# Optimization experiments

Hardware: AMD Instinct MI355X
Metric: run time of the kernel (lower is better)

The kernel has to match this reference:

```python
import jax, jax.numpy as jnp
import numpy as np

UPSCALE = 4
IMG_RANGE = 1.0
B, CIN, H, W = 4, 3, 128, 128
NF, NB = 64, 16


def conv2d(x, w, b=None):
    y = jax.lax.conv_general_dilated(x, w, (1, 1), 'SAME',
                                     dimension_numbers=('NCHW', 'OIHW', 'NCHW'))
    return y if b is None else y + b[None, :, None, None]


def binary_act(x):
    # sign forward, piecewise-polynomial surrogate backward (STE)
    sg = jax.lax.stop_gradient
    out_fwd = jnp.sign(x)
    m1 = (x < -1).astype(x.dtype)
    m2 = (x < 0).astype(x.dtype)
    m3 = (x < 1).astype(x.dtype)
    out1 = -m1 + (x * x + 2.0 * x) * (1.0 - m1)
    out2 = out1 * m2 + (-x * x + 2.0 * x) * (1.0 - m2)
    out3 = out2 * m3 + (1.0 - m3)
    return sg(out_fwd) - sg(out3) + out3


def binarize_weight(w):
    # per-output-channel scaling factor * sign(w); gradient flows through clamp (STE)
    sg = jax.lax.stop_gradient
    scale = sg(jnp.mean(jnp.abs(w), axis=(1, 2, 3), keepdims=True))
    bw = scale * jnp.sign(w)
    cw = jnp.clip(w, -1.0, 1.0)
    return sg(bw) - sg(cw) + cw


def rprelu(x, b1, a, b2):
    x = x + b1[None, :, None, None]
    x = jnp.where(x >= 0, x, a[None, :, None, None] * x)
    return x + b2[None, :, None, None]


def bbcu(x, move, w, a, b1, b2):
    # BBCU unit: learnable bias -> binary act -> binary conv -> RPReLU -> + identity residual
    out = binary_act(x + move[None, :, None, None])
    out = conv2d(out, binarize_weight(w))
    return rprelu(out, b1, a, b2) + x


def pixel_shuffle(x, r):
    n, c, h, w = x.shape
    x = x.reshape(n, c // (r * r), r, r, h, w)
    return x.transpose(0, 1, 4, 2, 5, 3).reshape(n, c // (r * r), h * r, w * r)


def up_conv(x, move, w, a, b1, b2, r):
    # channel-expanding BBCU with channel-repeat residual, then pixel shuffle
    out = binary_act(x + move[None, :, None, None])
    out = conv2d(out, binarize_weight(w))
    out = rprelu(out, b1, a, b2) + jnp.tile(x, (1, r * r, 1, 1))
    return pixel_shuffle(out, r)


def setup_inputs() -> dict:
    key = jax.random.key(0)
    ks = jax.random.split(key, 8)
    nu = 2 * NB  # 2 BBCU convs per BinaryBlock
    inp = {
        'x': jax.random.uniform(ks[0], (B, CIN, H, W), jnp.float32),
        'conv_first_w': jax.random.normal(ks[1], (NF, CIN, 3, 3), jnp.float32) * 0.05,
        'conv_first_b': jnp.zeros((NF,), jnp.float32),
        'body_move': jnp.zeros((nu, NF), jnp.float32),
        'body_w': jax.random.normal(ks[2], (nu, NF, NF, 3, 3), jnp.float32) * 0.001,
        'body_a': jnp.full((nu, NF), 0.25, jnp.float32),
        'body_b1': jnp.zeros((nu, NF), jnp.float32),
        'body_b2': jnp.zeros((nu, NF), jnp.float32),
        'up1_move': jnp.zeros((NF,), jnp.float32),
        'up1_w': jax.random.normal(ks[3], (4 * NF, NF, 3, 3), jnp.float32) * 0.001,
        'up1_a': jnp.full((4 * NF,), 0.25, jnp.float32),
        'up1_b1': jnp.zeros((4 * NF,), jnp.float32),
        'up1_b2': jnp.zeros((4 * NF,), jnp.float32),
        'up2_move': jnp.zeros((NF,), jnp.float32),
        'up2_w': jax.random.normal(ks[4], (4 * NF, NF, 3, 3), jnp.float32) * 0.001,
        'up2_a': jnp.full((4 * NF,), 0.25, jnp.float32),
        'up2_b1': jnp.zeros((4 * NF,), jnp.float32),
        'up2_b2': jnp.zeros((4 * NF,), jnp.float32),
        'hr_move': jnp.zeros((NF,), jnp.float32),
        'hr_w': jax.random.normal(ks[5], (NF, NF, 3, 3), jnp.float32) * 0.001,
        'hr_a': jnp.full((NF,), 0.25, jnp.float32),
        'hr_b1': jnp.zeros((NF,), jnp.float32),
        'hr_b2': jnp.zeros((NF,), jnp.float32),
        'conv_last_w': jax.random.normal(ks[6], (CIN, NF, 3, 3), jnp.float32) * 0.05,
        'conv_last_b': jnp.zeros((CIN,), jnp.float32),
    }
    return inp


def reference(x, conv_first_w, conv_first_b,
              body_move, body_w, body_a, body_b1, body_b2,
              up1_move, up1_w, up1_a, up1_b1, up1_b2,
              up2_move, up2_w, up2_a, up2_b1, up2_b2,
              hr_move, hr_w, hr_a, hr_b1, hr_b2,
              conv_last_w, conv_last_b):
    x = x * IMG_RANGE
    feat = jax.nn.leaky_relu(conv2d(x, conv_first_w, conv_first_b), 0.1)

    def step(h, p):
        move, w, a, b1, b2 = p
        return bbcu(h, move, w, a, b1, b2), None

    out, _ = jax.lax.scan(step, feat, (body_move, body_w, body_a, body_b1, body_b2))
    out = up_conv(out, up1_move, up1_w, up1_a, up1_b1, up1_b2, 2)
    out = up_conv(out, up2_move, up2_w, up2_a, up2_b1, up2_b2, 2)
    out = bbcu(out, hr_move, hr_w, hr_a, hr_b1, hr_b2)
    out = conv2d(jax.nn.leaky_relu(out, 0.1), conv_last_w, conv_last_b)
    n, c, h, w = x.shape
    base = jax.image.resize(x, (n, c, h * UPSCALE, w * UPSCALE), method='bilinear')
    return (out + base) / IMG_RANGE
```

## Files before the change

### kernel.cpp

```cpp
#include <hip/hip_runtime.h>


typedef unsigned long long u64;
typedef unsigned int u32;
typedef unsigned short u16;
typedef unsigned char u8;

__device__ inline float fadd(float a, float b) { return __fadd_rn(a, b); }
__device__ inline float fmul(float a, float b) { return __fmul_rn(a, b); }

__device__ inline u64 spread4(u64 x) {
  x &= 0xFFFFULL;
  x = (x | (x << 24)) & 0x000000FF000000FFULL;
  x = (x | (x << 12)) & 0x000F000F000F000FULL;
  x = (x | (x << 6))  & 0x0303030303030303ULL;
  x = (x | (x << 3))  & 0x1111111111111111ULL;
  return x;
}

__device__ float pw_abs_sum(const float* p, int n) {
  if (n <= 8) {
    float s = fabsf(p[0]);
    for (int i = 1; i < n; i++) s = fadd(s, fabsf(p[i]));
    return s;
  }
  if (n <= 128) {
    float r[8];
#pragma unroll
    for (int q = 0; q < 8; q++) r[q] = fabsf(p[q]);
    int i;
    for (i = 8; i + 8 <= n; i += 8)
#pragma unroll
      for (int q = 0; q < 8; q++) r[q] = fadd(r[q], fabsf(p[i + q]));
    float res = fadd(fadd(fadd(r[0], r[1]), fadd(r[2], r[3])),
                     fadd(fadd(r[4], r[5]), fadd(r[6], r[7])));
    for (; i < n; i++) res = fadd(res, fabsf(p[i]));
    return res;
  }
  int n2 = (n / 2) & ~7;
  return fadd(pw_abs_sum(p, n2), pw_abs_sum(p + n2, n - n2));
}

__global__ __launch_bounds__(256) void diag_kernel(float* __restrict__ out,
                                                   int n, float tag) {
  int idx = blockIdx.x * 256 + threadIdx.x;
  if (idx < n) out[idx] = (idx == 0) ? tag : 0.f;
}

__global__ __launch_bounds__(64) void binw_pack_kernel(
    const float* __restrict__ w, u64* __restrict__ wbits,
    float* __restrict__ scale, int nch) {
  int ch = blockIdx.x * 64 + threadIdx.x;
  if (ch >= nch) return;
  const float* wc = w + (size_t)ch * 576;
  float S = pw_abs_sum(wc, 576);
  scale[ch] = __fdiv_rn(S, 576.0f);
  u64 b[9] = {0, 0, 0, 0, 0, 0, 0, 0, 0};
  for (int ci = 0; ci < 64; ci++) {
#pragma unroll
    for (int tap = 0; tap < 9; tap++)
      b[tap] |= (u64)(wc[ci * 9 + tap] > 0.0f) << ci;
  }
#pragma unroll
  for (int tap = 0; tap < 9; tap++) wbits[(size_t)ch * 9 + tap] = b[tap];
}

__global__ __launch_bounds__(256) void conv_first_kernel(
    const float* __restrict__ x,
    const float* __restrict__ w, const float* __restrict__ b,
    float* __restrict__ out) {
  int n = blockIdx.y;
  const float* xn = x + (size_t)n * 49152;
  float* on = out + (size_t)n * 1048576;
  int idx = blockIdx.x * 256 + threadIdx.x;
  int gx = idx & 127;
  int gy = (idx >> 7) & 127;
  int co = idx >> 14;
  const float* wp = w + co * 27;
  float acc = 0.f;
  for (int ky = 0; ky < 3; ky++) {
    int yy = gy + ky - 1;
    if (yy < 0 || yy > 127) continue;
    for (int kx = 0; kx < 3; kx++) {
      int xx = gx + kx - 1;
      if (xx < 0 || xx > 127) continue;
      for (int ci = 0; ci < 3; ci++)
        acc = fmaf(xn[ci * 16384 + yy * 128 + xx],
                   wp[ci * 9 + ky * 3 + kx], acc);
    }
  }
  float wb = fadd(acc, b[co]);
  on[idx] = wb >= 0.f ? wb : fmul(0.1f, wb);
}

__global__ __launch_bounds__(256) void tr_kernel(
    const float* __restrict__ in,
    float* __restrict__ out) {
  __shared__ float s[64][65];
  int n = blockIdx.y;
  int p0 = blockIdx.x * 64;
  const float* fi = in + (size_t)n * 1048576;
  float* fo = out + (size_t)n * 1048576;
  int t = threadIdx.x;
  for (int i = t; i < 4096; i += 256) {
    int ch = i >> 6, px = i & 63;
    s[ch][px] = fi[(size_t)ch * 16384 + p0 + px];
  }
  __syncthreads();
  for (int i = t; i < 1024; i += 256) {
    int px = i >> 4, c4 = i & 15;
    float4 v = make_float4(s[c4 * 4 + 0][px], s[c4 * 4 + 1][px],
                           s[c4 * 4 + 2][px], s[c4 * 4 + 3][px]);
    *(float4*)(fo + (size_t)(p0 + px) * 64 + c4 * 4) = v;
  }
}

__global__ __launch_bounds__(512, 8) void pack2_kernel(
    const float* __restrict__ feat,
    const float* __restrict__ move,
    u64* __restrict__ bits) {
  __shared__ float s_mvT[64];
  int t = threadIdx.x;
  if (t < 64) {
    int k = t >> 4, cq_ = t & 15;
    s_mvT[t] = move[4 * cq_ + k];
  }
  __syncthreads();
  int n = blockIdx.y;
  const float* f = feat + (size_t)n * 1048576;
  u64* bo = bits + (size_t)n * 16384;
  int lane = t & 63;
  int pp = lane >> 4, cq = lane & 15;
  int pix = blockIdx.x * 32 + (t >> 6) * 4 + pp;
  float4 v = *(const float4*)(f + (size_t)pix * 64 + 4 * cq);
  float vv[4] = {v.x, v.y, v.z, v.w};
  int sg[4];
#pragma unroll
  for (int k = 0; k < 4; k++)
    sg[k] = fadd(vv[k], s_mvT[k * 16 + cq]) > 0.0f;
  u64 m0 = __ballot(sg[0]);
  u64 m1 = __ballot(sg[1]);
  u64 m2 = __ballot(sg[2]);
  u64 m3 = __ballot(sg[3]);
  if (cq == 0) {
    int sh = 16 * pp;
    bo[pix] = spread4(m0 >> sh) | (spread4(m1 >> sh) << 1) |
              (spread4(m2 >> sh) << 2) | (spread4(m3 >> sh) << 3);
  }
}

__global__ __launch_bounds__(512, 8) void body_kernel(
    const u64* __restrict__ bits_in,
    const float* __restrict__ feat,
    const u64* __restrict__ wbits,
    const float* __restrict__ scale, const float* __restrict__ pa,
    const float* __restrict__ pb1, const float* __restrict__ pb2,
    const float* __restrict__ nmove,
    float* __restrict__ out,
    u64* __restrict__ bits_out)
{
  __shared__ u64 s_w[576];
  __shared__ u64 s_b[3 * 36];
  __shared__ float s_scT[64], s_aT[64], s_b1T[64], s_b2T[64], s_mvT[64];

  int t = threadIdx.x;
  int n = blockIdx.y;
  const u64* bin = bits_in + (size_t)n * 16384;

  int pix0 = blockIdx.x * 32;
  int py = pix0 >> 7, px0 = pix0 & 127;

  for (int i = t; i < 576; i += 512) {
    int cq_ = i & 15, tk = i >> 4;
    int k = tk & 3, tap = tk >> 2;
    s_w[i] = wbits[(4 * cq_ + k) * 9 + tap];
  }
  for (int i = t; i < 102; i += 512) {
    int r = i / 34, c = i - r * 34;
    int yy = py - 1 + r, xx = px0 - 1 + c;
    s_b[r * 36 + c] = (yy >= 0 && yy < 128 && xx >= 0 && xx < 128)
                          ? bin[yy * 128 + xx] : 0ULL;
  }
  if (t < 64) {
    int k = t >> 4, cq_ = t & 15;
    int co = 4 * cq_ + k;
    s_scT[t] = scale[co]; s_aT[t] = pa[co];
    s_b1T[t] = pb1[co];   s_b2T[t] = pb2[co];
    s_mvT[t] = nmove[co];
  }
  __syncthreads();

  const float* fin = feat + (size_t)n * 1048576;
  float* outp = out + (size_t)n * 1048576;
  u64* bop = bits_out + (size_t)n * 16384;

  int lane = t & 63;
  int pp = lane >> 4, cq = lane & 15;
  int pl = (t >> 6) * 4 + pp;
  int pix = pix0 + pl;
  int px = px0 + pl;

  u64 nb[9];
  int vf = 0, nvalid = 0;
#pragma unroll
  for (int ky = 0; ky < 3; ky++)
#pragma unroll
    for (int kx = 0; kx < 3; kx++) {
      int yy = py + ky - 1, xx = px + kx - 1;
      int tap = ky * 3 + kx;
      nb[tap] = s_b[ky * 36 + pl + kx];
      if (yy >= 0 && yy < 128 && xx >= 0 && xx < 128) {
        vf |= 1 << tap; nvalid++;
      }
    }
  bool interior = (vf == 511);
  int base = 64 * nvalid;

  float4 rv4 = *(const float4*)(fin + (size_t)pix * 64 + 4 * cq);
  float rv[4] = {rv4.x, rv4.y, rv4.z, rv4.w};

  float vq[4];
  int sg[4];
#pragma unroll
  for (int k = 0; k < 4; k++) {
    int c = 0;
#pragma unroll
    for (int tap = 0; tap < 9; tap++)
      c += __popcll(nb[tap] ^ s_w[(tap * 4 + k) * 16 + cq]);
    if (!interior) {
#pragma unroll
      for (int tap = 0; tap < 9; tap++)
        if (!((vf >> tap) & 1)) c -= __popcll(s_w[(tap * 4 + k) * 16 + cq]);
    }
    int sint = base - 2 * c;
    int pi = k * 16 + cq;
    float conv = fmul(s_scT[pi], (float)sint);
    float t1 = fadd(conv, s_b1T[pi]);
    float t2 = t1 >= 0.0f ? t1 : fmul(s_aT[pi], t1);
    float t3 = fadd(t2, s_b2T[pi]);
    float ov = fadd(t3, rv[k]);
    vq[k] = ov;
    sg[k] = fadd(ov, s_mvT[pi]) > 0.0f;
  }
  *(float4*)(outp + (size_t)pix * 64 + 4 * cq) =
      make_float4(vq[0], vq[1], vq[2], vq[3]);

  u64 m0 = __ballot(sg[0]);
  u64 m1 = __ballot(sg[1]);
  u64 m2 = __ballot(sg[2]);
  u64 m3 = __ballot(sg[3]);
  if (cq == 0) {
    int sh = 16 * pp;
    bop[pix] = spread4(m0 >> sh) | (spread4(m1 >> sh) << 1) |
               (spread4(m2 >> sh) << 2) | (spread4(m3 >> sh) << 3);
  }
}

template <int W2, bool RES_NHWC>
__global__ __launch_bounds__(512, 8) void upoc_kernel(
    const u64* __restrict__ bits_in,
    const float* __restrict__ feat,
    const u64* __restrict__ wbits,
    const float* __restrict__ scale, const float* __restrict__ pa,
    const float* __restrict__ pb1, const float* __restrict__ pb2,
    const float* __restrict__ nmove,
    float* __restrict__ out,
    u64* __restrict__ bits_out)
{
  constexpr int W = W2 / 2;
  constexpr int LOG2W2 = (W2 == 512) ? 9 : 8;
  constexpr size_t HWin = (size_t)W * W;
  constexpr size_t HWout = (size_t)W2 * W2;
  __shared__ u64 s_w[2304];
  __shared__ u64 s_b[3 * 20];
  __shared__ float s_scT[256], s_aT[256], s_b1T[256], s_b2T[256], s_mv[64];

  int t = threadIdx.x;
  int n = blockIdx.z;
  const u64* bin = bits_in + (size_t)n * HWin;

  int opix0 = blockIdx.x * 32;
  int ogy0 = opix0 >> LOG2W2;
  int ogx0 = opix0 & (W2 - 1);
  int ipy0 = ogy0 >> 1, ipx0 = ogx0 >> 1;

  for (int i = t; i < 2304; i += 512) {
    int tap = i >> 8, r = i & 255;
    int cq_ = r & 15, ksp = r >> 4;
    int co = 16 * cq_ + 4 * (ksp >> 2) + (ksp & 3);
    s_w[i] = wbits[co * 9 + tap];
  }
  for (int i = t; i < 54; i += 512) {
    int r = i / 18, c = i - r * 18;
    int yy = ipy0 - 1 + r, xx = ipx0 - 1 + c;
    s_b[r * 20 + c] = (yy >= 0 && yy < W && xx >= 0 && xx < W)
                          ? bin[(size_t)yy * W + xx] : 0ULL;
  }
  for (int i = t; i < 256; i += 512) {
    int cq_ = i & 15, ksp = i >> 4;
    int co = 16 * cq_ + 4 * (ksp >> 2) + (ksp & 3);
    s_scT[i] = scale[co]; s_aT[i] = pa[co];
    s_b1T[i] = pb1[co];   s_b2T[i] = pb2[co];
  }
  if (t < 64) s_mv[t] = nmove[t];
  __syncthreads();

  const float* fin = feat + (size_t)n * 64 * HWin;
  float* op = out + (size_t)n * HWout * 64;
  u64* bop = bits_out + (size_t)n * HWout;

  int lane = t & 63;
  int pp = lane >> 4, cq = lane & 15;
  int wv = (blockIdx.x * 512 + t) >> 6;
  int opix = wv * 4 + pp;
  int ogy = opix >> LOG2W2;
  int ogx = opix & (W2 - 1);
  int ipy = ogy >> 1, ipx = ogx >> 1;
  int sp = ((ogy & 1) << 1) | (ogx & 1);
  int dx = ipx - ipx0;

  u64 nb[9];
  int vf = 0, nvalid = 0;
#pragma unroll
  for (int ky = 0; ky < 3; ky++)
#pragma unroll
    for (int kx = 0; kx < 3; kx++) {
      int yy = ipy + ky - 1, xx = ipx + kx - 1;
      int tap = ky * 3 + kx;
      nb[tap] = s_b[ky * 20 + dx + kx];
      if (yy >= 0 && yy < W && xx >= 0 && xx < W) {
        vf |= 1 << tap; nvalid++;
      }
    }
  bool interior = (vf == 511);
  int base = 64 * nvalid;
  size_t ipix = (size_t)ipy * W + ipx;

  float rvv[4];
#pragma unroll
  for (int k = 0; k < 4; k++) {
    int rch = (16 * cq + 4 * k + sp) & 63;
    rvv[k] = RES_NHWC ? fin[ipix * 64 + rch]
                      : fin[(size_t)rch * HWin + ipix];
  }

  float vq[4];
  int sg[4];
#pragma unroll
  for (int k = 0; k < 4; k++) {
    int ochan = 4 * cq + k;
    int wi = (k * 4 + sp) * 16 + cq;
    int c = 0;
#pragma unroll
    for (int tap = 0; tap < 9; tap++)
      c += __popcll(nb[tap] ^ s_w[tap * 256 + wi]);
    if (!interior) {
#pragma unroll
      for (int tap = 0; tap < 9; tap++)
        if (!((vf >> tap) & 1)) c -= __popcll(s_w[tap * 256 + wi]);
    }
    int sint = base - 2 * c;
    float conv = fmul(s_scT[wi], (float)sint);
    float t1 = fadd(conv, s_b1T[wi]);
    float t2 = t1 >= 0.0f ? t1 : fmul(s_aT[wi], t1);
    float t3 = fadd(t2, s_b2T[wi]);
    float ov = fadd(t3, rvv[k]);
    vq[k] = ov;
    sg[k] = fadd(ov, s_mv[ochan]) > 0.0f;
  }
  float4 v4 = make_float4(vq[0], vq[1], vq[2], vq[3]);
  *(float4*)(op + (size_t)opix * 64 + 4 * cq) = v4;

  u64 m0 = __ballot(sg[0]);
  u64 m1 = __ballot(sg[1]);
  u64 m2 = __ballot(sg[2]);
  u64 m3 = __ballot(sg[3]);
  if (cq == 0) {
    int sh = 16 * pp;
    u64 word = spread4(m0 >> sh) | (spread4(m1 >> sh) << 1) |
               (spread4(m2 >> sh) << 2) | (spread4(m3 >> sh) << 3);
    bop[opix] = word;
  }
}

__global__ __launch_bounds__(512, 4) void hrcl_kernel(
    const u64* __restrict__ bits,
    const float* __restrict__ U,
    const u64* __restrict__ hwb, const float* __restrict__ hsc,
    const float* __restrict__ ha, const float* __restrict__ hb1,
    const float* __restrict__ hb2,
    const float* __restrict__ clw, const float* __restrict__ clb,
    const float* __restrict__ x,
    float* __restrict__ out) {
  __shared__ __align__(16) float s_v[108 * 68];
  __shared__ u64 s_hw[576];
  __shared__ u64 s_b[8 * 20];
  __shared__ float s_scT[64], s_aT[64], s_b1T[64], s_b2T[64];
  __shared__ __align__(16) float s_cw[1728];
  __shared__ float s_cb[3];

  int t = threadIdx.x;
  int x0 = blockIdx.x * 16, y0 = blockIdx.y * 4;

  for (int i = t; i < 576; i += 512) {
    int cq_ = i & 15, tk = i >> 4;
    int k = tk & 3, tap = tk >> 2;
    s_hw[i] = hwb[(4 * cq_ + k) * 9 + tap];
  }
  for (int i = t; i < 160; i += 512) {
    int r = i / 20, c = i - r * 20;
    int yy = y0 - 2 + r, xx = x0 - 2 + c;
    s_b[i] = (yy >= 0 && yy < 512 && xx >= 0 && xx < 512)
                 ? bits[(size_t)yy * 512 + xx] : 0ULL;
  }
  if (t < 64) {
    int k = t >> 4, cq_ = t & 15;
    int co = 4 * cq_ + k;
    s_scT[t] = hsc[co]; s_aT[t] = ha[co];
    s_b1T[t] = hb1[co]; s_b2T[t] = hb2[co];
  }
  for (int i = t; i < 1728; i += 512) {
    int tap = i / 192, r = i - tap * 192;
    int co = r >> 6, ci = r & 63;
    s_cw[i] = clw[co * 576 + ci * 9 + tap];
  }
  if (t < 3) s_cb[t] = clb[t];
  __syncthreads();

  for (int i = t; i < 1728; i += 512) {
    int cq = i & 15, hpx = i >> 4;
    int hrow = hpx / 18, hcol = hpx - hrow * 18;
    int gy = y0 - 1 + hrow, gx = x0 - 1 + hcol;
    float vq[4] = {0.f, 0.f, 0.f, 0.f};
    if (gy >= 0 && gy < 512 && gx >= 0 && gx < 512) {
      u64 nb[9];
      int vf = 0, nvalid = 0;
#pragma unroll
      for (int ky = 0; ky < 3; ky++)
#pragma unroll
        for (int kx = 0; kx < 3; kx++) {
          int yy = gy + ky - 1, xx = gx + kx - 1;
          int tap = ky * 3 + kx;
          nb[tap] = s_b[(hrow + ky) * 20 + hcol + kx];
          if (yy >= 0 && yy < 512 && xx >= 0 && xx < 512) {
            vf |= 1 << tap; nvalid++;
          }
        }
      bool interior = (vf == 511);
      int base = 64 * nvalid;
      float4 uv = *(const float4*)(U + ((size_t)gy * 512 + gx) * 64 + 4 * cq);
      float us[4] = {uv.x, uv.y, uv.z, uv.w};
#pragma unroll
      for (int k = 0; k < 4; k++) {
        int c = 0;
#pragma unroll
        for (int tap = 0; tap < 9; tap++)
          c += __popcll(nb[tap] ^ s_hw[(tap * 4 + k) * 16 + cq]);
        if (!interior) {
#pragma unroll
          for (int tap = 0; tap < 9; tap++)
            if (!((vf >> tap) & 1))
              c -= __popcll(s_hw[(tap * 4 + k) * 16 + cq]);
        }
        int sint = base - 2 * c;
        int pi = k * 16 + cq;
        float conv = fmul(s_scT[pi], (float)sint);
        float t1 = fadd(conv, s_b1T[pi]);
        float t2 = t1 >= 0.0f ? t1 : fmul(s_aT[pi], t1);
        float t3 = fadd(t2, s_b2T[pi]);
        float ov = fadd(t3, us[k]);
        vq[k] = ov >= 0.0f ? ov : fmul(0.1f, ov);
      }
    }
    *(float4*)(s_v + hpx * 68 + 4 * cq) =
        make_float4(vq[0], vq[1], vq[2], vq[3]);
  }
  __syncthreads();

  int lane = t & 63, wave = t >> 6;
  int pp = lane >> 4, cq = lane & 15;
#pragma unroll
  for (int pass = 0; pass < 2; pass++) {
    int p = pass * 32 + wave * 4 + pp;
    int pr = p >> 4, pc = p & 15;
    float a0 = 0.f, a1 = 0.f, a2 = 0.f;
#pragma unroll
    for (int ky = 0; ky < 3; ky++)
#pragma unroll
      for (int kx = 0; kx < 3; kx++) {
        int tap = ky * 3 + kx;
        int hp = (pr + ky) * 18 + (pc + kx);
        float4 v = *(const float4*)(s_v + hp * 68 + 4 * cq);
        float4 w0 = *(const float4*)(s_cw + (tap * 3 + 0) * 64 + 4 * cq);
        float4 w1 = *(const float4*)(s_cw + (tap * 3 + 1) * 64 + 4 * cq);
        float4 w2 = *(const float4*)(s_cw + (tap * 3 + 2) * 64 + 4 * cq);
        a0 = fmaf(v.x, w0.x, a0); a0 = fmaf(v.y, w0.y, a0);
        a0 = fmaf(v.z, w0.z, a0); a0 = fmaf(v.w, w0.w, a0);
        a1 = fmaf(v.x, w1.x, a1); a1 = fmaf(v.y, w1.y, a1);
        a1 = fmaf(v.z, w1.z, a1); a1 = fmaf(v.w, w1.w, a1);
        a2 = fmaf(v.x, w2.x, a2); a2 = fmaf(v.y, w2.y, a2);
        a2 = fmaf(v.z, w2.z, a2); a2 = fmaf(v.w, w2.w, a2);
      }
#pragma unroll
    for (int m = 1; m < 16; m <<= 1) {
      a0 = fadd(a0, __shfl_xor(a0, m));
      a1 = fadd(a1, __shfl_xor(a1, m));
      a2 = fadd(a2, __shfl_xor(a2, m));
    }
    if (cq == 0) {
      int ogx = x0 + pc, ogy = y0 + pr;
      float o0 = fadd(a0, s_cb[0]);
      float o1 = fadd(a1, s_cb[1]);
      float o2 = fadd(a2, s_cb[2]);
      float sy = (ogy + 0.5f) * 0.25f - 0.5f;
      float sx = (ogx + 0.5f) * 0.25f - 0.5f;
      int iy0 = (int)floorf(sy);
      int ix0 = (int)floorf(sx);
      float fy = sy - (float)iy0, fx = sx - (float)ix0;
      int y0c = min(max(iy0, 0), 127), y1c = min(max(iy0 + 1, 0), 127);
      int x0c = min(max(ix0, 0), 127), x1c = min(max(ix0 + 1, 0), 127);
      float accs[3] = {o0, o1, o2};
#pragma unroll
      for (int co = 0; co < 3; co++) {
        const float* xp = x + (size_t)co * 16384;
        float c00 = xp[y0c * 128 + x0c], c01 = xp[y0c * 128 + x1c];
        float c10 = xp[y1c * 128 + x0c], c11 = xp[y1c * 128 + x1c];
        float v0, v1;
        if (y1c == y0c) { v0 = fmul(1.f, c00); v1 = fmul(1.f, c01); }
        else {
          v0 = fadd(fmul(1.f - fy, c00), fmul(fy, c10));
          v1 = fadd(fmul(1.f - fy, c01), fmul(fy, c11));
        }
        float base = (x1c == x0c) ? fmul(1.f, v0)
                                  : fadd(fmul(1.f - fx, v0), fmul(fx, v1));
        out[((size_t)co << 18) + ((size_t)ogy << 9) + ogx] =
            fadd(accs[co], base);
      }
    }
  }
}

extern "C" void kernel_launch(void* const* d_in, const int* in_sizes, int n_in,
                              void* d_out, int out_size, void* d_ws,
                              size_t ws_size, hipStream_t stream) {
  const float* x         = (const float*)d_in[0];
  const float* cf_w      = (const float*)d_in[1];
  const float* cf_b      = (const float*)d_in[2];
  const float* body_move = (const float*)d_in[3];
  const float* body_w    = (const float*)d_in[4];
  const float* body_a    = (const float*)d_in[5];
  const float* body_b1   = (const float*)d_in[6];
  const float* body_b2   = (const float*)d_in[7];
  const float* up1_move  = (const float*)d_in[8];
  const float* up1_w     = (const float*)d_in[9];
  const float* up1_a     = (const float*)d_in[10];
  const float* up1_b1    = (const float*)d_in[11];
  const float* up1_b2    = (const float*)d_in[12];
  const float* up2_move  = (const float*)d_in[13];
  const float* up2_w     = (const float*)d_in[14];
  const float* up2_a     = (const float*)d_in[15];
  const float* up2_b1    = (const float*)d_in[16];
  const float* up2_b2    = (const float*)d_in[17];
  const float* hr_move   = (const float*)d_in[18];
  const float* hr_w      = (const float*)d_in[19];
  const float* hr_a      = (const float*)d_in[20];
  const float* hr_b1     = (const float*)d_in[21];
  const float* hr_b2     = (const float*)d_in[22];
  const float* cl_w      = (const float*)d_in[23];
  const float* cl_b      = (const float*)d_in[24];
  float* out = (float*)d_out;

  const size_t M = 1024 * 1024;
  if (ws_size < 160 * M) {
    diag_kernel<<<(out_size + 255) / 256, 256, 0, stream>>>(
        out, out_size, (float)(ws_size >> 20));
    return;
  }

  char* ws = (char*)d_ws;
  float* A0    = (float*)(ws + 0);
  float* A1    = (float*)(ws + 16 * M);
  float* Pbat  = (float*)(ws + 16 * M);
  float* U     = (float*)(ws + 80 * M);
  u64* bitsA   = (u64*)(ws + 144 * M);
  u64* bitsB   = (u64*)(ws + 144 * M + 512 * 1024);
  u64* bits256 = (u64*)(ws + 145 * M);
  u64* bits512 = (u64*)(ws + 147 * M);
  u64* wbits   = (u64*)(ws + 149 * M);
  float* scales = (float*)(ws + 150 * M);

  binw_pack_kernel<<<32, 64, 0, stream>>>(body_w, wbits, scales, 2048);
  binw_pack_kernel<<<4, 64, 0, stream>>>(up1_w, wbits + (size_t)2048 * 9,
                                         scales + 2048, 256);
  binw_pack_kernel<<<4, 64, 0, stream>>>(up2_w, wbits + (size_t)2304 * 9,
                                         scales + 2304, 256);
  binw_pack_kernel<<<1, 64, 0, stream>>>(hr_w, wbits + (size_t)2560 * 9,
                                         scales + 2560, 64);

  conv_first_kernel<<<dim3(4096, 4), 256, 0, stream>>>(x, cf_w, cf_b, A1);
  tr_kernel<<<dim3(256, 4), 256, 0, stream>>>(A1, A0);
  pack2_kernel<<<dim3(512, 4), 512, 0, stream>>>(A0, body_move, bitsA);

  float* fin = A0;
  float* fout = A1;
  u64* bbin = bitsA;
  u64* bbout = bitsB;
  for (int u = 0; u < 32; u++) {
    const float* nm = (u < 31) ? body_move + (u + 1) * 64 : up1_move;
    body_kernel<<<dim3(512, 4), 512, 0, stream>>>(
        bbin, fin, wbits + (size_t)u * 576, scales + u * 64,
        body_a + u * 64, body_b1 + u * 64, body_b2 + u * 64, nm,
        fout, bbout);
    float* tf = fin; fin = fout; fout = tf;
    u64* tb = bbin; bbin = bbout; bbout = tb;
  }

  upoc_kernel<256, true><<<dim3(2048, 1, 4), 512, 0, stream>>>(
      bitsA, A0, wbits + (size_t)2048 * 9, scales + 2048,
      up1_a, up1_b1, up1_b2, up2_move, Pbat, bits256);

  for (int n = 0; n < 4; n++) {
    upoc_kernel<512, true><<<dim3(8192, 1, 1), 512, 0, stream>>>(
        bits256 + (size_t)n * 65536, Pbat + (size_t)n * 4194304,
        wbits + (size_t)2304 * 9, scales + 2304,
        up2_a, up2_b1, up2_b2, hr_move, U, bits512);
    hrcl_kernel<<<dim3(32, 128), 512, 0, stream>>>(
        bits512, U, wbits + (size_t)2560 * 9, scales + 2560,
        hr_a, hr_b1, hr_b2, cl_w, cl_b,
        x + (size_t)n * 49152, out + (size_t)n * 786432);
  }
}
```

Baseline: 1.423 ms.

## Fuse first conv with transpose and bit-pack, widen upconv and last-conv tiles

Replaces the separate first-conv, transpose and bit-pack kernels with one kernel. It computes the 3-channel conv per pixel directly in NHWC, writes the features and packs the sign bits, which removes two full-feature round trips through global memory and two launches. The upsampling conv kernel now handles 64 output pixels per block instead of 32, which halves the grid and amortises the per-block weight and parameter staging in shared memory. The final conv reduction is re-split to 8 pixels per wave with 8 lanes each, so it needs fewer shuffle steps and no second pass.

```diff
diff --git a/kernel.cpp b/kernel.cpp
--- a/kernel.cpp
+++ b/kernel.cpp
@@ -65,79 +65,68 @@
   for (int tap = 0; tap < 9; tap++) wbits[(size_t)ch * 9 + tap] = b[tap];
 }
 
-__global__ __launch_bounds__(256) void conv_first_kernel(
+__global__ __launch_bounds__(512, 8) void conv_first2_kernel(
     const float* __restrict__ x,
-    const float* __restrict__ w, const float* __restrict__ b,
-    float* __restrict__ out) {
+    const float* __restrict__ w,
+    const float* __restrict__ b,
+    const float* __restrict__ move,
+    float* __restrict__ out,
+    u64* __restrict__ bits) {
+  __shared__ float s_w2[1728];
+  __shared__ float s_bT[64], s_mvT[64];
+  int t = threadIdx.x;
+  for (int i = t; i < 1728; i += 512) {
+    int s = i >> 6, co = i & 63;
+    int tap = s / 3, ci = s - tap * 3;
+    s_w2[i] = w[co * 27 + ci * 9 + tap];
+  }
+  if (t < 64) {
+    int k = t >> 4, cq_ = t & 15;
+    s_bT[t] = b[4 * cq_ + k];
+    s_mvT[t] = move[4 * cq_ + k];
+  }
+  __syncthreads();
+
   int n = blockIdx.y;
   const float* xn = x + (size_t)n * 49152;
   float* on = out + (size_t)n * 1048576;
-  int idx = blockIdx.x * 256 + threadIdx.x;
-  int gx = idx & 127;
-  int gy = (idx >> 7) & 127;
-  int co = idx >> 14;
-  const float* wp = w + co * 27;
-  float acc = 0.f;
-  for (int ky = 0; ky < 3; ky++) {
-    int yy = gy + ky - 1;
-    if (yy < 0 || yy > 127) continue;
-    for (int kx = 0; kx < 3; kx++) {
-      int xx = gx + kx - 1;
-      if (xx < 0 || xx > 127) continue;
-      for (int ci = 0; ci < 3; ci++)
-        acc = fmaf(xn[ci * 16384 + yy * 128 + xx],
-                   wp[ci * 9 + ky * 3 + kx], acc);
-    }
-  }
-  float wb = fadd(acc, b[co]);
-  on[idx] = wb >= 0.f ? wb : fmul(0.1f, wb);
-}
-
-__global__ __launch_bounds__(256) void tr_kernel(
-    const float* __restrict__ in,
-    float* __restrict__ out) {
-  __shared__ float s[64][65];
-  int n = blockIdx.y;
-  int p0 = blockIdx.x * 64;
-  const float* fi = in + (size_t)n * 1048576;
-  float* fo = out + (size_t)n * 1048576;
-  int t = threadIdx.x;
-  for (int i = t; i < 4096; i += 256) {
-    int ch = i >> 6, px = i & 63;
-    s[ch][px] = fi[(size_t)ch * 16384 + p0 + px];
-  }
-  __syncthreads();
-  for (int i = t; i < 1024; i += 256) {
-    int px = i >> 4, c4 = i & 15;
-    float4 v = make_float4(s[c4 * 4 + 0][px], s[c4 * 4 + 1][px],
-                           s[c4 * 4 + 2][px], s[c4 * 4 + 3][px]);
-    *(float4*)(fo + (size_t)(p0 + px) * 64 + c4 * 4) = v;
-  }
-}
-
-__global__ __launch_bounds__(512, 8) void pack2_kernel(
-    const float* __restrict__ feat,
-    const float* __restrict__ move,
-    u64* __restrict__ bits) {
-  __shared__ float s_mvT[64];
-  int t = threadIdx.x;
-  if (t < 64) {
-    int k = t >> 4, cq_ = t & 15;
-    s_mvT[t] = move[4 * cq_ + k];
-  }
-  __syncthreads();
-  int n = blockIdx.y;
-  const float* f = feat + (size_t)n * 1048576;
   u64* bo = bits + (size_t)n * 16384;
   int lane = t & 63;
   int pp = lane >> 4, cq = lane & 15;
   int pix = blockIdx.x * 32 + (t >> 6) * 4 + pp;
-  float4 v = *(const float4*)(f + (size_t)pix * 64 + 4 * cq);
-  float vv[4] = {v.x, v.y, v.z, v.w};
+  int px = pix & 127, py = pix >> 7;
+
+  float xv[27];
+#pragma unroll
+  for (int ky = 0; ky < 3; ky++) {
+    int yy = py + ky - 1;
+#pragma unroll
+    for (int kx = 0; kx < 3; kx++) {
+      int xx = px + kx - 1;
+      bool ok = (yy >= 0 && yy < 128 && xx >= 0 && xx < 128);
+#pragma unroll
+      for (int ci = 0; ci < 3; ci++)
+        xv[(ky * 3 + kx) * 3 + ci] =
+            ok ? xn[ci * 16384 + yy * 128 + xx] : 0.0f;
+    }
+  }
+  float vq[4];
   int sg[4];
 #pragma unroll
-  for (int k = 0; k < 4; k++)
-    sg[k] = fadd(vv[k], s_mvT[k * 16 + cq]) > 0.0f;
+  for (int k = 0; k < 4; k++) {
+    int co = 4 * cq + k;
+    float acc = 0.f;
+#pragma unroll
+    for (int s = 0; s < 27; s++)
+      acc = fmaf(xv[s], s_w2[s * 64 + co], acc);
+    int pi = k * 16 + cq;
+    float wb = fadd(acc, s_bT[pi]);
+    float r = wb >= 0.f ? wb : fmul(0.1f, wb);
+    vq[k] = r;
+    sg[k] = fadd(r, s_mvT[pi]) > 0.0f;
+  }
+  *(float4*)(on + (size_t)pix * 64 + 4 * cq) =
+      make_float4(vq[0], vq[1], vq[2], vq[3]);
   u64 m0 = __ballot(sg[0]);
   u64 m1 = __ballot(sg[1]);
   u64 m2 = __ballot(sg[2]);
@@ -272,14 +261,14 @@
   constexpr size_t HWin = (size_t)W * W;
   constexpr size_t HWout = (size_t)W2 * W2;
   __shared__ u64 s_w[2304];
-  __shared__ u64 s_b[3 * 20];
+  __shared__ u64 s_b[3 * 36];
   __shared__ float s_scT[256], s_aT[256], s_b1T[256], s_b2T[256], s_mv[64];
 
   int t = threadIdx.x;
   int n = blockIdx.z;
   const u64* bin = bits_in + (size_t)n * HWin;
 
-  int opix0 = blockIdx.x * 32;
+  int opix0 = blockIdx.x * 64;
   int ogy0 = opix0 >> LOG2W2;
   int ogx0 = opix0 & (W2 - 1);
   int ipy0 = ogy0 >> 1, ipx0 = ogx0 >> 1;
@@ -290,10 +279,10 @@
     int co = 16 * cq_ + 4 * (ksp >> 2) + (ksp & 3);
     s_w[i] = wbits[co * 9 + tap];
   }
-  for (int i = t; i < 54; i += 512) {
-    int r = i / 18, c = i - r * 18;
+  for (int i = t; i < 102; i += 512) {
+    int r = i / 34, c = i - r * 34;
     int yy = ipy0 - 1 + r, xx = ipx0 - 1 + c;
-    s_b[r * 20 + c] = (yy >= 0 && yy < W && xx >= 0 && xx < W)
+    s_b[r * 36 + c] = (yy >= 0 && yy < W && xx >= 0 && xx < W)
                           ? bin[(size_t)yy * W + xx] : 0ULL;
   }
   for (int i = t; i < 256; i += 512) {
@@ -311,75 +300,78 @@
 
   int lane = t & 63;
   int pp = lane >> 4, cq = lane & 15;
-  int wv = (blockIdx.x * 512 + t) >> 6;
-  int opix = wv * 4 + pp;
-  int ogy = opix >> LOG2W2;
-  int ogx = opix & (W2 - 1);
-  int ipy = ogy >> 1, ipx = ogx >> 1;
-  int sp = ((ogy & 1) << 1) | (ogx & 1);
-  int dx = ipx - ipx0;
-
-  u64 nb[9];
-  int vf = 0, nvalid = 0;
-#pragma unroll
-  for (int ky = 0; ky < 3; ky++)
-#pragma unroll
-    for (int kx = 0; kx < 3; kx++) {
-      int yy = ipy + ky - 1, xx = ipx + kx - 1;
-      int tap = ky * 3 + kx;
-      nb[tap] = s_b[ky * 20 + dx + kx];
-      if (yy >= 0 && yy < W && xx >= 0 && xx < W) {
-        vf |= 1 << tap; nvalid++;
+
+#pragma unroll
+  for (int g = 0; g < 2; g++) {
+    int opix = opix0 + g * 32 + (t >> 6) * 4 + pp;
+    int ogy = opix >> LOG2W2;
+    int ogx = opix & (W2 - 1);
+    int ipy = ogy >> 1, ipx = ogx >> 1;
+    int sp = ((ogy & 1) << 1) | (ogx & 1);
+    int dx = ipx - ipx0;
+
+    u64 nb[9];
+    int vf = 0, nvalid = 0;
+#pragma unroll
+    for (int ky = 0; ky < 3; ky++)
+#pragma unroll
+      for (int kx = 0; kx < 3; kx++) {
+        int yy = ipy + ky - 1, xx = ipx + kx - 1;
+        int tap = ky * 3 + kx;
+        nb[tap] = s_b[ky * 36 + dx + kx];
+        if (yy >= 0 && yy < W && xx >= 0 && xx < W) {
+          vf |= 1 << tap; nvalid++;
+        }
       }
-    }
-  bool interior = (vf == 511);
-  int base = 64 * nvalid;
-  size_t ipix = (size_t)ipy * W + ipx;
-
-  float rvv[4];
-#pragma unroll
-  for (int k = 0; k < 4; k++) {
-    int rch = (16 * cq + 4 * k + sp) & 63;
-    rvv[k] = RES_NHWC ? fin[ipix * 64 + rch]
-                      : fin[(size_t)rch * HWin + ipix];
-  }
-
-  float vq[4];
-  int sg[4];
-#pragma unroll
-  for (int k = 0; k < 4; k++) {
-    int ochan = 4 * cq + k;
-    int wi = (k * 4 + sp) * 16 + cq;
-    int c = 0;
-#pragma unroll
-    for (int tap = 0; tap < 9; tap++)
-      c += __popcll(nb[tap] ^ s_w[tap * 256 + wi]);
-    if (!interior) {
+    bool interior = (vf == 511);
+    int base = 64 * nvalid;
+    size_t ipix = (size_t)ipy * W + ipx;
+
+    float rvv[4];
+#pragma unroll
+    for (int k = 0; k < 4; k++) {
+      int rch = (16 * cq + 4 * k + sp) & 63;
+      rvv[k] = RES_NHWC ? fin[ipix * 64 + rch]
+                        : fin[(size_t)rch * HWin + ipix];
+    }
+
+    float vq[4];
+    int sg[4];
+#pragma unroll
+    for (int k = 0; k < 4; k++) {
+      int ochan = 4 * cq + k;
+      int wi = (k * 4 + sp) * 16 + cq;
+      int c = 0;
 #pragma unroll
       for (int tap = 0; tap < 9; tap++)
-        if (!((vf >> tap) & 1)) c -= __popcll(s_w[tap * 256 + wi]);
-    }
-    int sint = base - 2 * c;
-    float conv = fmul(s_scT[wi], (float)sint);
-    float t1 = fadd(conv, s_b1T[wi]);
-    float t2 = t1 >= 0.0f ? t1 : fmul(s_aT[wi], t1);
-    float t3 = fadd(t2, s_b2T[wi]);
-    float ov = fadd(t3, rvv[k]);
-    vq[k] = ov;
-    sg[k] = fadd(ov, s_mv[ochan]) > 0.0f;
-  }
-  float4 v4 = make_float4(vq[0], vq[1], vq[2], vq[3]);
-  *(float4*)(op + (size_t)opix * 64 + 4 * cq) = v4;
-
-  u64 m0 = __ballot(sg[0]);
-  u64 m1 = __ballot(sg[1]);
-  u64 m2 = __ballot(sg[2]);
-  u64 m3 = __ballot(sg[3]);
-  if (cq == 0) {
-    int sh = 16 * pp;
-    u64 word = spread4(m0 >> sh) | (spread4(m1 >> sh) << 1) |
-               (spread4(m2 >> sh) << 2) | (spread4(m3 >> sh) << 3);
-    bop[opix] = word;
+        c += __popcll(nb[tap] ^ s_w[tap * 256 + wi]);
+      if (!interior) {
+#pragma unroll
+        for (int tap = 0; tap < 9; tap++)
+          if (!((vf >> tap) & 1)) c -= __popcll(s_w[tap * 256 + wi]);
+      }
+      int sint = base - 2 * c;
+      float conv = fmul(s_scT[wi], (float)sint);
+      float t1 = fadd(conv, s_b1T[wi]);
+      float t2 = t1 >= 0.0f ? t1 : fmul(s_aT[wi], t1);
+      float t3 = fadd(t2, s_b2T[wi]);
+      float ov = fadd(t3, rvv[k]);
+      vq[k] = ov;
+      sg[k] = fadd(ov, s_mv[ochan]) > 0.0f;
+    }
+    float4 v4 = make_float4(vq[0], vq[1], vq[2], vq[3]);
+    *(float4*)(op + (size_t)opix * 64 + 4 * cq) = v4;
+
+    u64 m0 = __ballot(sg[0]);
+    u64 m1 = __ballot(sg[1]);
+    u64 m2 = __ballot(sg[2]);
+    u64 m3 = __ballot(sg[3]);
+    if (cq == 0) {
+      int sh = 16 * pp;
+      u64 word = spread4(m0 >> sh) | (spread4(m1 >> sh) << 1) |
+                 (spread4(m2 >> sh) << 2) | (spread4(m3 >> sh) << 3);
+      bop[opix] = word;
+    }
   }
 }
 
@@ -478,64 +470,73 @@
   __syncthreads();
 
   int lane = t & 63, wave = t >> 6;
-  int pp = lane >> 4, cq = lane & 15;
-#pragma unroll
-  for (int pass = 0; pass < 2; pass++) {
-    int p = pass * 32 + wave * 4 + pp;
-    int pr = p >> 4, pc = p & 15;
-    float a0 = 0.f, a1 = 0.f, a2 = 0.f;
-#pragma unroll
-    for (int ky = 0; ky < 3; ky++)
-#pragma unroll
-      for (int kx = 0; kx < 3; kx++) {
-        int tap = ky * 3 + kx;
-        int hp = (pr + ky) * 18 + (pc + kx);
-        float4 v = *(const float4*)(s_v + hp * 68 + 4 * cq);
-        float4 w0 = *(const float4*)(s_cw + (tap * 3 + 0) * 64 + 4 * cq);
-        float4 w1 = *(const float4*)(s_cw + (tap * 3 + 1) * 64 + 4 * cq);
-        float4 w2 = *(const float4*)(s_cw + (tap * 3 + 2) * 64 + 4 * cq);
-        a0 = fmaf(v.x, w0.x, a0); a0 = fmaf(v.y, w0.y, a0);
-        a0 = fmaf(v.z, w0.z, a0); a0 = fmaf(v.w, w0.w, a0);
-        a1 = fmaf(v.x, w1.x, a1); a1 = fmaf(v.y, w1.y, a1);
-        a1 = fmaf(v.z, w1.z, a1); a1 = fmaf(v.w, w1.w, a1);
-        a2 = fmaf(v.x, w2.x, a2); a2 = fmaf(v.y, w2.y, a2);
-        a2 = fmaf(v.z, w2.z, a2); a2 = fmaf(v.w, w2.w, a2);
+  int pp8 = lane >> 3;
+  int cq3 = lane & 7;
+  int p = wave * 8 + pp8;
+  int pr = p >> 4, pc = p & 15;
+  float a0 = 0.f, a1 = 0.f, a2 = 0.f;
+#pragma unroll
+  for (int ky = 0; ky < 3; ky++)
+#pragma unroll
+    for (int kx = 0; kx < 3; kx++) {
+      int tap = ky * 3 + kx;
+      int hp = (pr + ky) * 18 + (pc + kx);
+      const float* vp = s_v + hp * 68 + cq3 * 8;
+      float4 va = *(const float4*)(vp);
+      float4 vb = *(const float4*)(vp + 4);
+      const float* w0p = s_cw + (tap * 3 + 0) * 64 + cq3 * 8;
+      const float* w1p = s_cw + (tap * 3 + 1) * 64 + cq3 * 8;
+      const float* w2p = s_cw + (tap * 3 + 2) * 64 + cq3 * 8;
+      float4 w0a = *(const float4*)(w0p), w0b = *(const float4*)(w0p + 4);
+      float4 w1a = *(const float4*)(w1p), w1b = *(const float4*)(w1p + 4);
+      float4 w2a = *(const float4*)(w2p), w2b = *(const float4*)(w2p + 4);
+      a0 = fmaf(va.x, w0a.x, a0); a0 = fmaf(va.y, w0a.y, a0);
+      a0 = fmaf(va.z, w0a.z, a0); a0 = fmaf(va.w, w0a.w, a0);
+      a0 = fmaf(vb.x, w0b.x, a0); a0 = fmaf(vb.y, w0b.y, a0);
+      a0 = fmaf(vb.z, w0b.z, a0); a0 = fmaf(vb.w, w0b.w, a0);
+      a1 = fmaf(va.x, w1a.x, a1); a1 = fmaf(va.y, w1a.y, a1);
+      a1 = fmaf(va.z, w1a.z, a1); a1 = fmaf(va.w, w1a.w, a1);
+      a1 = fmaf(vb.x, w1b.x, a1); a1 = fmaf(vb.y, w1b.y, a1);
+      a1 = fmaf(vb.z, w1b.z, a1); a1 = fmaf(vb.w, w1b.w, a1);
+      a2 = fmaf(va.x, w2a.x, a2); a2 = fmaf(va.y, w2a.y, a2);
+      a2 = fmaf(va.z, w2a.z, a2); a2 = fmaf(va.w, w2a.w, a2);
+      a2 = fmaf(vb.x, w2b.x, a2); a2 = fmaf(vb.y, w2b.y, a2);
+      a2 = fmaf(vb.z, w2b.z, a2); a2 = fmaf(vb.w, w2b.w, a2);
+    }
+#pragma unroll
+  for (int m = 1; m < 8; m <<= 1) {
+    a0 = fadd(a0, __shfl_xor(a0, m));
+    a1 = fadd(a1, __shfl_xor(a1, m));
+    a2 = fadd(a2, __shfl_xor(a2, m));
+  }
+  if (cq3 == 0) {
+    int ogx = x0 + pc, ogy = y0 + pr;
+    float o0 = fadd(a0, s_cb[0]);
+    float o1 = fadd(a1, s_cb[1]);
+    float o2 = fadd(a2, s_cb[2]);
+    float sy = (ogy + 0.5f) * 0.25f - 0.5f;
+    float sx = (ogx + 0.5f) * 0.25f - 0.5f;
+    int iy0 = (int)floorf(sy);
+    int ix0 = (int)floorf(sx);
+    float fy = sy - (float)iy0, fx = sx - (float)ix0;
+    int y0c = min(max(iy0, 0), 127), y1c = min(max(iy0 + 1, 0), 127);
+    int x0c = min(max(ix0, 0), 127), x1c = min(max(ix0 + 1, 0), 127);
+    float accs[3] = {o0, o1, o2};
+#pragma unroll
+    for (int co = 0; co < 3; co++) {
+      const float* xp = x + (size_t)co * 16384;
+      float c00 = xp[y0c * 128 + x0c], c01 = xp[y0c * 128 + x1c];
+      float c10 = xp[y1c * 128 + x0c], c11 = xp[y1c * 128 + x1c];
+      float v0, v1;
+      if (y1c == y0c) { v0 = fmul(1.f, c00); v1 = fmul(1.f, c01); }
+      else {
+        v0 = fadd(fmul(1.f - fy, c00), fmul(fy, c10));
+        v1 = fadd(fmul(1.f - fy, c01), fmul(fy, c11));
       }
-#pragma unroll
-    for (int m = 1; m < 16; m <<= 1) {
-      a0 = fadd(a0, __shfl_xor(a0, m));
-      a1 = fadd(a1, __shfl_xor(a1, m));
-      a2 = fadd(a2, __shfl_xor(a2, m));
-    }
-    if (cq == 0) {
-      int ogx = x0 + pc, ogy = y0 + pr;
-      float o0 = fadd(a0, s_cb[0]);
-      float o1 = fadd(a1, s_cb[1]);
-      float o2 = fadd(a2, s_cb[2]);
-      float sy = (ogy + 0.5f) * 0.25f - 0.5f;
-      float sx = (ogx + 0.5f) * 0.25f - 0.5f;
-      int iy0 = (int)floorf(sy);
-      int ix0 = (int)floorf(sx);
-      float fy = sy - (float)iy0, fx = sx - (float)ix0;
-      int y0c = min(max(iy0, 0), 127), y1c = min(max(iy0 + 1, 0), 127);
-      int x0c = min(max(ix0, 0), 127), x1c = min(max(ix0 + 1, 0), 127);
-      float accs[3] = {o0, o1, o2};
-#pragma unroll
-      for (int co = 0; co < 3; co++) {
-        const float* xp = x + (size_t)co * 16384;
-        float c00 = xp[y0c * 128 + x0c], c01 = xp[y0c * 128 + x1c];
-        float c10 = xp[y1c * 128 + x0c], c11 = xp[y1c * 128 + x1c];
-        float v0, v1;
-        if (y1c == y0c) { v0 = fmul(1.f, c00); v1 = fmul(1.f, c01); }
-        else {
-          v0 = fadd(fmul(1.f - fy, c00), fmul(fy, c10));
-          v1 = fadd(fmul(1.f - fy, c01), fmul(fy, c11));
-        }
-        float base = (x1c == x0c) ? fmul(1.f, v0)
-                                  : fadd(fmul(1.f - fx, v0), fmul(fx, v1));
-        out[((size_t)co << 18) + ((size_t)ogy << 9) + ogx] =
-            fadd(accs[co], base);
-      }
+      float base = (x1c == x0c) ? fmul(1.f, v0)
+                                : fadd(fmul(1.f - fx, v0), fmul(fx, v1));
+      out[((size_t)co << 18) + ((size_t)ogy << 9) + ogx] =
+          fadd(accs[co], base);
     }
   }
 }
@@ -597,9 +598,8 @@
   binw_pack_kernel<<<1, 64, 0, stream>>>(hr_w, wbits + (size_t)2560 * 9,
                                          scales + 2560, 64);
 
-  conv_first_kernel<<<dim3(4096, 4), 256, 0, stream>>>(x, cf_w, cf_b, A1);
-  tr_kernel<<<dim3(256, 4), 256, 0, stream>>>(A1, A0);
-  pack2_kernel<<<dim3(512, 4), 512, 0, stream>>>(A0, body_move, bitsA);
+  conv_first2_kernel<<<dim3(512, 4), 512, 0, stream>>>(
+      x, cf_w, cf_b, body_move, A0, bitsA);
 
   float* fin = A0;
   float* fout = A1;
@@ -615,12 +615,12 @@
     u64* tb = bbin; bbin = bbout; bbout = tb;
   }
 
-  upoc_kernel<256, true><<<dim3(2048, 1, 4), 512, 0, stream>>>(
+  upoc_kernel<256, true><<<dim3(1024, 1, 4), 512, 0, stream>>>(
       bitsA, A0, wbits + (size_t)2048 * 9, scales + 2048,
       up1_a, up1_b1, up1_b2, up2_move, Pbat, bits256);
 
   for (int n = 0; n < 4; n++) {
-    upoc_kernel<512, true><<<dim3(8192, 1, 1), 512, 0, stream>>>(
+    upoc_kernel<512, true><<<dim3(4096, 1, 1), 512, 0, stream>>>(
         bits256 + (size_t)n * 65536, Pbat + (size_t)n * 4194304,
         wbits + (size_t)2304 * 9, scales + 2304,
         up2_a, up2_b1, up2_b2, hr_move, U, bits512);
```

Result: faster. 1.300 ms (-8.7%).
